# Optimization experiments

Hardware: AMD Instinct MI355X
Metric: run time of the kernel (lower is better)

Reference implementation:

```python
import jax, jax.numpy as jnp
import numpy as np

DT_RANK = 12


def _mixer(x, in_w, conv_w, conv_b, xproj_w, dt_w, dt_b, A_log, D_skip, out_w):
    # x: [B, L, d_model]
    B, L, _ = x.shape
    d_inner, d_state = A_log.shape
    k = conv_w.shape[-1]
    xz = x @ in_w.T                                  # [B, L, 2*d_inner]
    x_part, z = jnp.split(xz, 2, axis=-1)
    # causal depthwise conv1d (torch pads both sides with k-1 then slices [:L] == left-pad only)
    xc = x_part.transpose(0, 2, 1)                   # [B, d_inner, L]
    xc = jax.lax.conv_general_dilated(
        xc, conv_w, window_strides=(1,), padding=[(k - 1, 0)],
        feature_group_count=d_inner, dimension_numbers=("NCH", "OIH", "NCH"))
    xc = xc + conv_b[None, :, None]
    x_part = jax.nn.silu(xc.transpose(0, 2, 1))      # [B, L, d_inner]
    dt_bc = x_part @ xproj_w.T                       # [B, L, dt_rank + 2*d_state]
    dt_part = dt_bc[..., :DT_RANK]
    b_term = jnp.tanh(dt_bc[..., DT_RANK:DT_RANK + d_state])
    c_term = jnp.tanh(dt_bc[..., DT_RANK + d_state:])
    dt = jax.nn.softplus(dt_part @ dt_w.T + dt_b) + 1e-4   # [B, L, d_inner]
    a = -jnp.exp(A_log)                              # [d_inner, d_state]

    def step(state, inp):
        x_t, dt_t, b_t, c_t = inp                    # [B,di], [B,di], [B,N], [B,N]
        da = jnp.exp(dt_t[:, :, None] * a)           # [B, di, N]
        db = (1.0 - da) * b_t[:, None, :]
        state = da * state + db * x_t[:, :, None]
        y_t = (state * c_t[:, None, :]).sum(-1) + D_skip * x_t
        return state, y_t

    init = jnp.zeros((B, d_inner, d_state), x.dtype)
    xs = (x_part.transpose(1, 0, 2), dt.transpose(1, 0, 2),
          b_term.transpose(1, 0, 2), c_term.transpose(1, 0, 2))
    _, ys = jax.lax.scan(step, init, xs)             # ys: [L, B, d_inner]
    y = ys.transpose(1, 0, 2) * jax.nn.silu(z)
    return y @ out_w.T                               # [B, L, d_model]


def setup_inputs() -> dict:
    key = jax.random.key(0)
    B, L, D = 32, 577, 192
    d_inner, d_state, d_conv = 384, 8, 4
    ks = jax.random.split(key, 16)
    s = 0.02
    inp = {"x": jax.random.normal(ks[0], (B, L, D), jnp.float32)}
    for i, p in enumerate(["fw", "bw"]):
        kk = jax.random.split(ks[1 + i], 8)
        inp[f"{p}_in_w"] = jax.random.normal(kk[0], (2 * d_inner, D), jnp.float32) * s
        inp[f"{p}_conv_w"] = jax.random.normal(kk[1], (d_inner, 1, d_conv), jnp.float32) * 0.1
        inp[f"{p}_conv_b"] = jnp.zeros((d_inner,), jnp.float32)
        inp[f"{p}_xproj_w"] = jax.random.normal(kk[2], (DT_RANK + 2 * d_state, d_inner), jnp.float32) * s
        inp[f"{p}_dt_w"] = jax.random.normal(kk[3], (d_inner, DT_RANK), jnp.float32) * s
        inp[f"{p}_dt_b"] = jnp.zeros((d_inner,), jnp.float32)
        inp[f"{p}_A_log"] = jax.random.uniform(kk[4], (d_inner, d_state), jnp.float32)
        inp[f"{p}_D"] = jnp.ones((d_inner,), jnp.float32)
        inp[f"{p}_out_w"] = jax.random.normal(kk[5], (D, d_inner), jnp.float32) * s
    return inp


def reference(x,
              fw_in_w, fw_conv_w, fw_conv_b, fw_xproj_w, fw_dt_w, fw_dt_b, fw_A_log, fw_D, fw_out_w,
              bw_in_w, bw_conv_w, bw_conv_b, bw_xproj_w, bw_dt_w, bw_dt_b, bw_A_log, bw_D, bw_out_w):
    y_fwd = _mixer(x, fw_in_w, fw_conv_w, fw_conv_b, fw_xproj_w, fw_dt_w, fw_dt_b, fw_A_log, fw_D, fw_out_w)
    x_rev = jnp.flip(x, axis=1)
    y_bwd = _mixer(x_rev, bw_in_w, bw_conv_w, bw_conv_b, bw_xproj_w, bw_dt_w, bw_dt_b, bw_A_log, bw_D, bw_out_w)
    y_bwd = jnp.flip(y_bwd, axis=1)
    return 0.5 * (y_fwd + y_bwd)
```

## Files before the change

### kernel.cpp

```cpp
#include <hip/hip_runtime.h>
#include <hip/hip_bf16.h>

#define L2E 1.44269504088896340f
#define LN2 0.69314718055994531f

typedef __bf16 bf16x8 __attribute__((ext_vector_type(8)));
typedef __bf16 bf16x4 __attribute__((ext_vector_type(4)));
typedef float f32x4 __attribute__((ext_vector_type(4)));

__device__ __forceinline__ float fexp2(float x){ return __builtin_amdgcn_exp2f(x); }
__device__ __forceinline__ float flog2(float x){ return __builtin_amdgcn_logf(x); }
__device__ __forceinline__ float frcp(float x){ return __builtin_amdgcn_rcpf(x); }
__device__ __forceinline__ float fsigmoid(float x){ return frcp(1.f + fexp2(-x*L2E)); }
__device__ __forceinline__ float fsoftplus(float x){
  float sp = flog2(1.f + fexp2(x*L2E))*LN2;
  return (x > 15.f) ? x : sp;
}
__device__ __forceinline__ float ftanh_(float x){
  x = fminf(fmaxf(x, -10.f), 10.f);
  float e = fexp2(2.f*L2E*x);
  return (e - 1.f)*frcp(e + 1.f);
}

#define NB 32
#define LS 577
#define DM 192
#define DI 384
#define BL 18464
#define M2T 36928
#define T_CH 37
#define N_CH 16

__global__ __launch_bounds__(256) void k_prep(
    const float* __restrict__ x,
    const float* __restrict__ fw_in, const float* __restrict__ bw_in,
    const float* __restrict__ fw_out, const float* __restrict__ bw_out,
    const float* __restrict__ fw_xp, const float* __restrict__ bw_xp,
    const float* __restrict__ fw_al, const float* __restrict__ bw_al,
    __hip_bfloat16* __restrict__ xbf, __hip_bfloat16* __restrict__ wcat,
    __hip_bfloat16* __restrict__ wout, __hip_bfloat16* __restrict__ xpp,
    float* __restrict__ alog2)
{
  const int S0 = 3545088;
  const int S1 = S0 + 294912;
  const int S2 = S1 + 147456;
  const int S3 = S2 + 24576;
  const int S4 = S3 + 6144;
  int idx = blockIdx.x*256 + threadIdx.x;
  if (idx < S0) {
    xbf[idx] = __float2bfloat16(x[idx]);
  } else if (idx < S1) {
    int i = idx - S0; int r = i/192, k = i - r*192;
    float v = (r < 768) ? fw_in[r*192+k] : bw_in[(r-768)*192+k];
    wcat[i] = __float2bfloat16(v);
  } else if (idx < S2) {
    int i = idx - S1; int o = i/768, k = i - o*768;
    float v = 0.5f * ((k < 384) ? fw_out[o*384+k] : bw_out[o*384+(k-384)]);
    wout[i] = __float2bfloat16(v);
  } else if (idx < S3) {
    int i = idx - S2; int d = i/12288; int rr = i - d*12288;
    int n = rr/384, k = rr - n*384;
    const float* xp = d ? bw_xp : fw_xp;
    float v = (n < 28) ? xp[n*384+k] : 0.f;
    xpp[i] = __float2bfloat16(v);
  } else if (idx < S4) {
    int i = idx - S3;
    const float* al = (i < 3072) ? fw_al : bw_al;
    int j = (i < 3072) ? i : (i - 3072);
    alog2[i] = -fexp2(al[j]*L2E) * L2E;
  }
}

#define G1_LDA 104
#define G1_LDO 136
__global__ __launch_bounds__(256) void k_gemm1(const __hip_bfloat16* __restrict__ A,
                                               const __hip_bfloat16* __restrict__ Bw,
                                               __hip_bfloat16* __restrict__ xg,
                                               __hip_bfloat16* __restrict__ zsb)
{
  __shared__ __align__(16) __bf16 smem[26624];
  __bf16* ldsA = smem;
  __bf16* ldsB = smem + 128*G1_LDA;

  const int t = threadIdx.x;
  const int tm = blockIdx.x / 12, tn = blockIdx.x - tm*12;
  const int m0 = tm*128, n0 = tn*128;
  const int w = t >> 6, lane = t & 63;
  const int wr = (w >> 1)*64, wc = (w & 1)*64;
  const int r = lane & 15, q = lane >> 4;

  f32x4 acc[4][4];
  #pragma unroll
  for (int a=0;a<4;++a)
    #pragma unroll
    for (int b=0;b<4;++b) acc[a][b] = (f32x4){0.f,0.f,0.f,0.f};

  #pragma unroll
  for (int h=0; h<2; ++h) {
    if (h) __syncthreads();
    #pragma unroll
    for (int j=0;j<6;++j) {
      int cid = t + 256*j;
      int row = cid/12; int c8 = (cid - row*12)*8;
      int gr = m0 + row; if (gr > BL-1) gr = BL-1;
      bf16x8 va = *(const bf16x8*)(A + (size_t)gr*192 + h*96 + c8);
      *(bf16x8*)(ldsA + row*G1_LDA + c8) = va;
      bf16x8 vb = *(const bf16x8*)(Bw + (size_t)(n0+row)*192 + h*96 + c8);
      *(bf16x8*)(ldsB + row*G1_LDA + c8) = vb;
    }
    __syncthreads();
    #pragma unroll
    for (int kc=0; kc<96; kc+=32) {
      bf16x8 af[4], bfv[4];
      #pragma unroll
      for (int mi=0; mi<4; ++mi)
        af[mi] = *(const bf16x8*)(ldsA + (wr + mi*16 + r)*G1_LDA + q*8 + kc);
      #pragma unroll
      for (int ni=0; ni<4; ++ni)
        bfv[ni] = *(const bf16x8*)(ldsB + (wc + ni*16 + r)*G1_LDA + q*8 + kc);
      #pragma unroll
      for (int mi=0; mi<4; ++mi)
        #pragma unroll
        for (int ni=0; ni<4; ++ni)
          acc[mi][ni] = __builtin_amdgcn_mfma_f32_16x16x32_bf16(af[mi], bfv[ni], acc[mi][ni], 0,0,0);
    }
  }

  const int cat = tn/3;
  const int cbase = (tn - cat*3)*128;
  const int d = cat >> 1, isz = cat & 1;
  __syncthreads();
  __bf16* ldsO = smem;
  #pragma unroll
  for (int mi=0; mi<4; ++mi)
    #pragma unroll
    for (int ni=0; ni<4; ++ni)
      #pragma unroll
      for (int rg=0; rg<4; ++rg) {
        int row = wr + mi*16 + q*4 + rg;
        int col = wc + ni*16 + r;
        float v = acc[mi][ni][rg];
        if (isz) v = v * fsigmoid(v);
        ldsO[row*G1_LDO + col] = (__bf16)v;
      }
  __syncthreads();
  __hip_bfloat16* dst = (isz ? zsb : xg) + (size_t)(d*BL)*384 + cbase;
  const int c8 = (t & 15)*8;
  #pragma unroll
  for (int it=0; it<8; ++it) {
    int row = (t >> 4) + it*16;
    int grow = m0 + row;
    if (grow < BL) {
      bf16x8 v = *(const bf16x8*)(ldsO + row*G1_LDO + c8);
      *(bf16x8*)(dst + (size_t)grow*384 + c8) = v;
    }
  }
}

__global__ __launch_bounds__(256) void k_conv(const __hip_bfloat16* __restrict__ xg,
                                              __hip_bfloat16* __restrict__ xcs,
                                              const float* __restrict__ fw_cw, const float* __restrict__ fw_cb,
                                              const float* __restrict__ bw_cw, const float* __restrict__ bw_cb)
{
  int idx = blockIdx.x*256 + threadIdx.x;
  int token = idx / 96; int g = idx - token*96; int c0 = g*4;
  int d = token / BL; int r2 = token - d*BL;
  int b = r2 / LS; int i = r2 - b*LS;
  const float* cwp = (d ? bw_cw : fw_cw);
  const float* cbp = (d ? bw_cb : fw_cb);
  f32x4 w0 = *(const f32x4*)(cwp + (c0+0)*4);
  f32x4 w1 = *(const f32x4*)(cwp + (c0+1)*4);
  f32x4 w2 = *(const f32x4*)(cwp + (c0+2)*4);
  f32x4 w3 = *(const f32x4*)(cwp + (c0+3)*4);
  f32x4 accv = *(const f32x4*)(cbp + c0);
  const __hip_bfloat16* base = xg + ((size_t)(d*BL + b*LS))*384 + c0;
  #pragma unroll
  for (int j=0;j<4;++j) {
    int iw = d ? (i+3-j) : (i-3+j);
    bool valid = d ? (iw < LS) : (iw >= 0);
    if (valid) {
      bf16x4 xv = *(const bf16x4*)(base + (size_t)iw*384);
      f32x4 wj = (f32x4){w0[j], w1[j], w2[j], w3[j]};
      #pragma unroll
      for (int ch=0; ch<4; ++ch) accv[ch] += wj[ch]*(float)xv[ch];
    }
  }
  bf16x4 outv;
  #pragma unroll
  for (int ch=0; ch<4; ++ch) {
    float s = accv[ch]*fsigmoid(accv[ch]);
    outv[ch] = (__bf16)s;
  }
  *(bf16x4*)(xcs + (size_t)token*384 + c0) = outv;
}

__global__ __launch_bounds__(256) void k_dtbc(const __hip_bfloat16* __restrict__ A,
                                              const __hip_bfloat16* __restrict__ xpp,
                                              float* __restrict__ dtbc)
{
  const int wid = blockIdx.x*4 + (threadIdx.x >> 6);
  if (wid >= 1154) return;
  const int lane = threadIdx.x & 63;
  const int m0 = wid*32;
  const int r = lane & 15, q = lane >> 4;
  const int d = (m0 >= BL) ? 1 : 0;
  const __hip_bfloat16* Bp = xpp + (size_t)d*32*384;
  f32x4 acc[2][2];
  #pragma unroll
  for (int a=0;a<2;++a)
    #pragma unroll
    for (int b=0;b<2;++b) acc[a][b] = (f32x4){0.f,0.f,0.f,0.f};
  const __hip_bfloat16* Ab = A + (size_t)(m0 + r)*384 + q*8;
  const __hip_bfloat16* Bb = Bp + (size_t)r*384 + q*8;
  #pragma unroll
  for (int kc = 0; kc < 384; kc += 32) {
    bf16x8 af0 = *(const bf16x8*)(Ab + kc);
    bf16x8 af1 = *(const bf16x8*)(Ab + 16*384 + kc);
    bf16x8 bf0 = *(const bf16x8*)(Bb + kc);
    bf16x8 bf1 = *(const bf16x8*)(Bb + 16*384 + kc);
    acc[0][0] = __builtin_amdgcn_mfma_f32_16x16x32_bf16(af0, bf0, acc[0][0], 0,0,0);
    acc[0][1] = __builtin_amdgcn_mfma_f32_16x16x32_bf16(af0, bf1, acc[0][1], 0,0,0);
    acc[1][0] = __builtin_amdgcn_mfma_f32_16x16x32_bf16(af1, bf0, acc[1][0], 0,0,0);
    acc[1][1] = __builtin_amdgcn_mfma_f32_16x16x32_bf16(af1, bf1, acc[1][1], 0,0,0);
  }
  #pragma unroll
  for (int mi=0; mi<2; ++mi)
    #pragma unroll
    for (int ni=0; ni<2; ++ni)
      #pragma unroll
      for (int rg=0; rg<4; ++rg) {
        int n = ni*16 + r;
        if (n < 28) {
          int m = m0 + mi*16 + q*4 + rg;
          float v = acc[mi][ni][rg];
          if (n >= 12) v = ftanh_(v);
          int r2 = m - d*BL; int b = r2 / LS; int i = r2 - b*LS;
          int ts = d ? (LS-1-i) : i;
          dtbc[((size_t)((d*NB + b)*LS + ts))*28 + n] = v;
        }
      }
}

__global__ __launch_bounds__(256) void k_dtfull(const float* __restrict__ dtbc,
                                                const float* __restrict__ fw_dtw, const float* __restrict__ fw_dtb,
                                                const float* __restrict__ bw_dtw, const float* __restrict__ bw_dtb,
                                                float* __restrict__ dtf)
{
  int idx = blockIdx.x*256 + threadIdx.x;
  int m = idx / 384; int c = idx - m*384;
  int d = (m >= BL) ? 1 : 0;
  const float* dtw = (d ? bw_dtw : fw_dtw) + c*12;
  float dtr = (d ? bw_dtb : fw_dtb)[c];
  const float* dp = dtbc + (size_t)m*28;
  #pragma unroll
  for (int r=0;r<12;++r) dtr += dp[r]*dtw[r];
  dtf[idx] = fsoftplus(dtr) + 1e-4f;
}

__global__ __launch_bounds__(64) void k_scan1(const __hip_bfloat16* __restrict__ xcs,
                                              const float* __restrict__ dtbc,
                                              const float* __restrict__ dtf,
                                              const float* __restrict__ alog2,
                                              float* __restrict__ ps)
{
  __shared__ __align__(16) float sB[T_CH*8];
  const int bid = blockIdx.x;
  const int lane = threadIdx.x;
  const int kc = bid & 15; const int dbc = bid >> 4;
  const int cchunk = dbc % 6; const int db = dbc / 6;
  const int b = db & 31; const int d = db >> 5;
  const int c = cchunk*64 + lane;

  const int ts0 = kc*T_CH;
  const int ts1 = (ts0 + T_CH < LS) ? (ts0 + T_CH) : LS;

  {
    const float* src = dtbc + ((size_t)((d*NB+b)*LS + ts0))*28;
    int n4 = (ts1 - ts0)*2;
    for (int j = lane; j < n4; j += 64)
      *(f32x4*)(sB + j*4) = *(const f32x4*)(src + (size_t)(j>>1)*28 + 12 + (j&1)*4);
  }

  float al[8];
  const float* alp = alog2 + ((size_t)(d*384 + c))*8;
  #pragma unroll
  for (int s=0;s<8;++s) al[s] = alp[s];

  const __hip_bfloat16* xcb = xcs + ((size_t)(d*BL + b*LS))*384 + c;
  const float* dfb = dtf + ((size_t)((d*NB+b)*LS))*384 + c;

  float P[8], S[8];
  #pragma unroll
  for (int s=0;s<8;++s){ P[s]=1.f; S[s]=0.f; }

  __syncthreads();

  float xnb, dtn;
  {
    int i = d ? (LS-1-ts0) : ts0;
    xnb = __bfloat162float(xcb[(size_t)i*384]);
    dtn = dfb[(size_t)ts0*384];
  }
  for (int ts=ts0; ts<ts1; ++ts) {
    f32x4 B0 = *(const f32x4*)(sB + (ts-ts0)*8);
    f32x4 B1 = *(const f32x4*)(sB + (ts-ts0)*8 + 4);
    float xt = xnb, dt = dtn;
    if (ts+1 < ts1) {
      int i2 = d ? (LS-2-ts) : (ts+1);
      xnb = __bfloat162float(xcb[(size_t)i2*384]);
      dtn = dfb[(size_t)(ts+1)*384];
    }
    #pragma unroll
    for (int s=0;s<8;++s) {
      float da = fexp2(dt * al[s]);
      float Bv = (s<4) ? B0[s] : B1[s-4];
      float tmp = Bv*xt;
      S[s] = tmp + da*(S[s]-tmp);
      P[s] *= da;
    }
  }
  float* pp = ps + ((size_t)bid*16)*64 + lane;
  #pragma unroll
  for (int s=0;s<8;++s) pp[s*64] = P[s];
  #pragma unroll
  for (int s=0;s<8;++s) pp[(8+s)*64] = S[s];
}

__global__ __launch_bounds__(64) void k_comb(const float* __restrict__ ps,
                                             float* __restrict__ initst)
{
  const int dbc = blockIdx.x;
  const int lane = threadIdx.x;
  float st[8];
  #pragma unroll
  for (int s=0;s<8;++s) st[s]=0.f;
  for (int kc=0;kc<N_CH;++kc) {
    const float* pp = ps + ((size_t)(dbc*N_CH+kc)*16)*64 + lane;
    float* ip = initst + ((size_t)(dbc*N_CH+kc)*8)*64 + lane;
    #pragma unroll
    for (int s=0;s<8;++s) ip[s*64] = st[s];
    #pragma unroll
    for (int s=0;s<8;++s) {
      float P = pp[s*64], Sv = pp[(8+s)*64];
      st[s] = P*st[s] + Sv;
    }
  }
}

__global__ __launch_bounds__(64) void k_scan2(const __hip_bfloat16* __restrict__ xcs,
                                              const __hip_bfloat16* __restrict__ zsb,
                                              const float* __restrict__ dtbc,
                                              const float* __restrict__ dtf,
                                              const float* __restrict__ initst,
                                              const float* __restrict__ fw_D,
                                              const float* __restrict__ bw_D,
                                              const float* __restrict__ alog2,
                                              __hip_bfloat16* __restrict__ ybf)
{
  __shared__ __align__(16) float sBC[T_CH*16];
  const int bid = blockIdx.x;
  const int lane = threadIdx.x;
  const int kc = bid & 15; const int dbc = bid >> 4;
  const int cchunk = dbc % 6; const int db = dbc / 6;
  const int b = db & 31; const int d = db >> 5;
  const int c = cchunk*64 + lane;

  const int ts0 = kc*T_CH;
  const int ts1 = (ts0 + T_CH < LS) ? (ts0 + T_CH) : LS;

  {
    const float* src = dtbc + ((size_t)((d*NB+b)*LS + ts0))*28;
    int n4 = (ts1 - ts0)*4;
    for (int j = lane; j < n4; j += 64)
      *(f32x4*)(sBC + j*4) = *(const f32x4*)(src + (size_t)(j>>2)*28 + 12 + (j&3)*4);
  }

  const float Dc  = (d ? bw_D : fw_D)[c];
  float al[8];
  const float* alp = alog2 + ((size_t)(d*384 + c))*8;
  #pragma unroll
  for (int s=0;s<8;++s) al[s] = alp[s];

  float st[8];
  {
    const float* ip = initst + ((size_t)bid*8)*64 + lane;
    #pragma unroll
    for (int s=0;s<8;++s) st[s] = ip[s*64];
  }

  const __hip_bfloat16* xcb = xcs + ((size_t)(d*BL + b*LS))*384 + c;
  const __hip_bfloat16* zcb = zsb + ((size_t)(d*BL + b*LS))*384 + c;
  const float* dfb = dtf + ((size_t)((d*NB+b)*LS))*384 + c;
  __hip_bfloat16* ybase = ybf + (size_t)(b*LS)*768 + d*384 + c;

  __syncthreads();

  float xnb, znb, dtn;
  {
    int i = d ? (LS-1-ts0) : ts0;
    xnb = __bfloat162float(xcb[(size_t)i*384]);
    znb = __bfloat162float(zcb[(size_t)i*384]);
    dtn = dfb[(size_t)ts0*384];
  }
  for (int ts=ts0; ts<ts1; ++ts) {
    f32x4 B0 = *(const f32x4*)(sBC + (ts-ts0)*16);
    f32x4 B1 = *(const f32x4*)(sBC + (ts-ts0)*16 + 4);
    f32x4 C0 = *(const f32x4*)(sBC + (ts-ts0)*16 + 8);
    f32x4 C1 = *(const f32x4*)(sBC + (ts-ts0)*16 + 12);
    float xt = xnb, zs = znb, dt = dtn;
    int i = d ? (LS-1-ts) : ts;
    if (ts+1 < ts1) {
      int i2 = d ? (LS-2-ts) : (ts+1);
      xnb = __bfloat162float(xcb[(size_t)i2*384]);
      znb = __bfloat162float(zcb[(size_t)i2*384]);
      dtn = dfb[(size_t)(ts+1)*384];
    }
    float y = Dc * xt;
    #pragma unroll
    for (int s=0;s<8;++s) {
      float da = fexp2(dt * al[s]);
      float Bv = (s<4) ? B0[s] : B1[s-4];
      float Cv = (s<4) ? C0[s] : C1[s-4];
      float tmp = Bv*xt;
      st[s] = tmp + da*(st[s]-tmp);
      y += st[s]*Cv;
    }
    ybase[(size_t)i*768] = __float2bfloat16(y*zs);
  }
}

__global__ __launch_bounds__(256) void k_gemm2(const __hip_bfloat16* __restrict__ A,
                                               const __hip_bfloat16* __restrict__ Bw,
                                               float* __restrict__ C)
{
  const int wid = blockIdx.x*4 + (threadIdx.x >> 6);
  if (wid >= 1731) return;
  const int lane = threadIdx.x & 63;
  const int tm = wid / 3, tn = wid - tm*3;
  const int m0 = tm*32, n0 = tn*64;
  const int r = lane & 15, q = lane >> 4;
  f32x4 acc[2][4];
  #pragma unroll
  for (int a=0;a<2;++a)
    #pragma unroll
    for (int b=0;b<4;++b) acc[a][b] = (f32x4){0.f,0.f,0.f,0.f};
  const __hip_bfloat16* Ab = A + (size_t)(m0 + r)*768 + q*8;
  const __hip_bfloat16* Bb = Bw + (size_t)(n0 + r)*768 + q*8;
  #pragma unroll 4
  for (int kc = 0; kc < 768; kc += 32) {
    bf16x8 af0 = *(const bf16x8*)(Ab + kc);
    bf16x8 af1 = *(const bf16x8*)(Ab + 16*768 + kc);
    bf16x8 bf0 = *(const bf16x8*)(Bb + kc);
    bf16x8 bf1 = *(const bf16x8*)(Bb + 16*768 + kc);
    bf16x8 bf2 = *(const bf16x8*)(Bb + 32*768 + kc);
    bf16x8 bf3 = *(const bf16x8*)(Bb + 48*768 + kc);
    acc[0][0] = __builtin_amdgcn_mfma_f32_16x16x32_bf16(af0, bf0, acc[0][0], 0,0,0);
    acc[0][1] = __builtin_amdgcn_mfma_f32_16x16x32_bf16(af0, bf1, acc[0][1], 0,0,0);
    acc[0][2] = __builtin_amdgcn_mfma_f32_16x16x32_bf16(af0, bf2, acc[0][2], 0,0,0);
    acc[0][3] = __builtin_amdgcn_mfma_f32_16x16x32_bf16(af0, bf3, acc[0][3], 0,0,0);
    acc[1][0] = __builtin_amdgcn_mfma_f32_16x16x32_bf16(af1, bf0, acc[1][0], 0,0,0);
    acc[1][1] = __builtin_amdgcn_mfma_f32_16x16x32_bf16(af1, bf1, acc[1][1], 0,0,0);
    acc[1][2] = __builtin_amdgcn_mfma_f32_16x16x32_bf16(af1, bf2, acc[1][2], 0,0,0);
    acc[1][3] = __builtin_amdgcn_mfma_f32_16x16x32_bf16(af1, bf3, acc[1][3], 0,0,0);
  }
  #pragma unroll
  for (int mi=0; mi<2; ++mi)
    #pragma unroll
    for (int ni=0; ni<4; ++ni)
      #pragma unroll
      for (int rg=0; rg<4; ++rg) {
        int row = m0 + mi*16 + q*4 + rg;
        int col = n0 + ni*16 + r;
        C[(size_t)row*192 + col] = acc[mi][ni][rg];
      }
}

extern "C" void kernel_launch(void* const* d_in, const int* in_sizes, int n_in,
                              void* d_out, int out_size, void* d_ws, size_t ws_size,
                              hipStream_t stream) {
  const float* x        = (const float*)d_in[0];
  const float* fw_in_w  = (const float*)d_in[1];
  const float* fw_cw    = (const float*)d_in[2];
  const float* fw_cb    = (const float*)d_in[3];
  const float* fw_xp    = (const float*)d_in[4];
  const float* fw_dtw   = (const float*)d_in[5];
  const float* fw_dtb   = (const float*)d_in[6];
  const float* fw_al    = (const float*)d_in[7];
  const float* fw_D     = (const float*)d_in[8];
  const float* fw_ow    = (const float*)d_in[9];
  const float* bw_in_w  = (const float*)d_in[10];
  const float* bw_cw    = (const float*)d_in[11];
  const float* bw_cb    = (const float*)d_in[12];
  const float* bw_xp    = (const float*)d_in[13];
  const float* bw_dtw   = (const float*)d_in[14];
  const float* bw_dtb   = (const float*)d_in[15];
  const float* bw_al    = (const float*)d_in[16];
  const float* bw_D     = (const float*)d_in[17];
  const float* bw_ow    = (const float*)d_in[18];

  char* ws = (char*)d_ws;
  __hip_bfloat16* wcat = (__hip_bfloat16*)(ws + 0);
  __hip_bfloat16* wout = (__hip_bfloat16*)(ws + 589824);
  __hip_bfloat16* xpp  = (__hip_bfloat16*)(ws + 884736);
  float* alog2         = (float*)(ws + 933888);
  __hip_bfloat16* xbf  = (__hip_bfloat16*)(ws + 958464);
  __hip_bfloat16* xg   = (__hip_bfloat16*)(ws + 8048640);
  float* initst        = (float*)(ws + 8048640);
  __hip_bfloat16* zsb  = (__hip_bfloat16*)(ws + 36409344);
  __hip_bfloat16* xcs  = (__hip_bfloat16*)(ws + 64770048);
  float* dtbc          = (float*)(ws + 93130752);
  float* dtf           = (float*)(ws + 97266688);
  float* ps            = (float*)(ws + 153988096);
  __hip_bfloat16* ybf  = (__hip_bfloat16*)(ws + 153988096);

  hipLaunchKernelGGL(k_prep, dim3(15696), dim3(256), 0, stream,
                     x, fw_in_w, bw_in_w, fw_ow, bw_ow, fw_xp, bw_xp, fw_al, bw_al,
                     xbf, wcat, wout, xpp, alog2);
  hipLaunchKernelGGL(k_gemm1, dim3(1740), dim3(256), 0, stream, xbf, wcat, xg, zsb);
  hipLaunchKernelGGL(k_conv, dim3(13848), dim3(256), 0, stream,
                     xg, xcs, fw_cw, fw_cb, bw_cw, bw_cb);
  hipLaunchKernelGGL(k_dtbc, dim3(289), dim3(256), 0, stream, xcs, xpp, dtbc);
  hipLaunchKernelGGL(k_dtfull, dim3(55392), dim3(256), 0, stream,
                     dtbc, fw_dtw, fw_dtb, bw_dtw, bw_dtb, dtf);
  hipLaunchKernelGGL(k_scan1, dim3(6144), dim3(64), 0, stream,
                     xcs, dtbc, dtf, alog2, ps);
  hipLaunchKernelGGL(k_comb, dim3(384), dim3(64), 0, stream, ps, initst);
  hipLaunchKernelGGL(k_scan2, dim3(6144), dim3(64), 0, stream,
                     xcs, zsb, dtbc, dtf, initst, fw_D, bw_D, alog2, ybf);
  hipLaunchKernelGGL(k_gemm2, dim3(433), dim3(256), 0, stream, ybf, wout, (float*)d_out);
}
```

Before: 323.9 us.

## Stage output GEMM tiles in LDS and vectorize dt projection over four channels

The output GEMM now has each 256-thread block load a 64-row A tile and the full 192-row weight tile into LDS in 96-wide K slices. Four waves then compute a 32x96 sub-tile each from shared memory, instead of every wave streaming its own operands from global memory. The dt-projection kernel now has each thread produce four channels with vector loads, so the shared dtbc row is read once and the launch needs a quarter of the threads. The trade-off is fewer GEMM blocks (289) with more LDS use and block-level barriers, plus clamped loads and guarded stores for the partial last tile.

```diff
diff --git a/kernel.cpp b/kernel.cpp
--- a/kernel.cpp
+++ b/kernel.cpp
@@ -247,14 +247,31 @@
                                                 float* __restrict__ dtf)
 {
   int idx = blockIdx.x*256 + threadIdx.x;
-  int m = idx / 384; int c = idx - m*384;
+  int m = idx / 96; int g = idx - m*96; int c0 = g*4;
   int d = (m >= BL) ? 1 : 0;
-  const float* dtw = (d ? bw_dtw : fw_dtw) + c*12;
-  float dtr = (d ? bw_dtb : fw_dtb)[c];
+  const float* dtw = (d ? bw_dtw : fw_dtw);
+  const float* dtbp = (d ? bw_dtb : fw_dtb);
   const float* dp = dtbc + (size_t)m*28;
-  #pragma unroll
-  for (int r=0;r<12;++r) dtr += dp[r]*dtw[r];
-  dtf[idx] = fsoftplus(dtr) + 1e-4f;
+  f32x4 p0 = *(const f32x4*)(dp);
+  f32x4 p1 = *(const f32x4*)(dp+4);
+  f32x4 p2 = *(const f32x4*)(dp+8);
+  f32x4 acc = *(const f32x4*)(dtbp + c0);
+  #pragma unroll
+  for (int ch=0; ch<4; ++ch) {
+    const float* wv = dtw + (size_t)(c0+ch)*12;
+    f32x4 w0 = *(const f32x4*)(wv);
+    f32x4 w1 = *(const f32x4*)(wv+4);
+    f32x4 w2 = *(const f32x4*)(wv+8);
+    float s = acc[ch];
+    #pragma unroll
+    for (int r=0;r<4;++r) s += p0[r]*w0[r];
+    #pragma unroll
+    for (int r=0;r<4;++r) s += p1[r]*w1[r];
+    #pragma unroll
+    for (int r=0;r<4;++r) s += p2[r]*w2[r];
+    acc[ch] = fsoftplus(s) + 1e-4f;
+  }
+  *(f32x4*)(dtf + (size_t)m*384 + c0) = acc;
 }
 
 __global__ __launch_bounds__(64) void k_scan1(const __hip_bfloat16* __restrict__ xcs,
@@ -429,49 +446,70 @@
   }
 }
 
+#define G2_LDA 104
 __global__ __launch_bounds__(256) void k_gemm2(const __hip_bfloat16* __restrict__ A,
                                                const __hip_bfloat16* __restrict__ Bw,
                                                float* __restrict__ C)
 {
-  const int wid = blockIdx.x*4 + (threadIdx.x >> 6);
-  if (wid >= 1731) return;
-  const int lane = threadIdx.x & 63;
-  const int tm = wid / 3, tn = wid - tm*3;
-  const int m0 = tm*32, n0 = tn*64;
+  __shared__ __align__(16) __bf16 smem[26624];
+  __bf16* ldsA = smem;
+  __bf16* ldsB = smem + 64*G2_LDA;
+
+  const int t = threadIdx.x;
+  const int m0 = blockIdx.x*64;
+  const int w = t >> 6, lane = t & 63;
+  const int wr = (w >> 1)*32, wc = (w & 1)*96;
   const int r = lane & 15, q = lane >> 4;
-  f32x4 acc[2][4];
+
+  f32x4 acc[2][6];
   #pragma unroll
   for (int a=0;a<2;++a)
     #pragma unroll
-    for (int b=0;b<4;++b) acc[a][b] = (f32x4){0.f,0.f,0.f,0.f};
-  const __hip_bfloat16* Ab = A + (size_t)(m0 + r)*768 + q*8;
-  const __hip_bfloat16* Bb = Bw + (size_t)(n0 + r)*768 + q*8;
-  #pragma unroll 4
-  for (int kc = 0; kc < 768; kc += 32) {
-    bf16x8 af0 = *(const bf16x8*)(Ab + kc);
-    bf16x8 af1 = *(const bf16x8*)(Ab + 16*768 + kc);
-    bf16x8 bf0 = *(const bf16x8*)(Bb + kc);
-    bf16x8 bf1 = *(const bf16x8*)(Bb + 16*768 + kc);
-    bf16x8 bf2 = *(const bf16x8*)(Bb + 32*768 + kc);
-    bf16x8 bf3 = *(const bf16x8*)(Bb + 48*768 + kc);
-    acc[0][0] = __builtin_amdgcn_mfma_f32_16x16x32_bf16(af0, bf0, acc[0][0], 0,0,0);
-    acc[0][1] = __builtin_amdgcn_mfma_f32_16x16x32_bf16(af0, bf1, acc[0][1], 0,0,0);
-    acc[0][2] = __builtin_amdgcn_mfma_f32_16x16x32_bf16(af0, bf2, acc[0][2], 0,0,0);
-    acc[0][3] = __builtin_amdgcn_mfma_f32_16x16x32_bf16(af0, bf3, acc[0][3], 0,0,0);
-    acc[1][0] = __builtin_amdgcn_mfma_f32_16x16x32_bf16(af1, bf0, acc[1][0], 0,0,0);
-    acc[1][1] = __builtin_amdgcn_mfma_f32_16x16x32_bf16(af1, bf1, acc[1][1], 0,0,0);
-    acc[1][2] = __builtin_amdgcn_mfma_f32_16x16x32_bf16(af1, bf2, acc[1][2], 0,0,0);
-    acc[1][3] = __builtin_amdgcn_mfma_f32_16x16x32_bf16(af1, bf3, acc[1][3], 0,0,0);
-  }
+    for (int b=0;b<6;++b) acc[a][b] = (f32x4){0.f,0.f,0.f,0.f};
+
+  #pragma unroll 1
+  for (int h=0; h<8; ++h) {
+    if (h) __syncthreads();
+    #pragma unroll
+    for (int j=0;j<3;++j) {
+      int cid = t + 256*j;
+      int row = cid/12; int c8 = (cid - row*12)*8;
+      int gr = m0 + row; if (gr > BL-1) gr = BL-1;
+      *(bf16x8*)(ldsA + row*G2_LDA + c8) = *(const bf16x8*)(A + (size_t)gr*768 + h*96 + c8);
+    }
+    #pragma unroll
+    for (int j=0;j<9;++j) {
+      int cid = t + 256*j;
+      int row = cid/12; int c8 = (cid - row*12)*8;
+      *(bf16x8*)(ldsB + row*G2_LDA + c8) = *(const bf16x8*)(Bw + (size_t)row*768 + h*96 + c8);
+    }
+    __syncthreads();
+    #pragma unroll
+    for (int kc=0; kc<96; kc+=32) {
+      bf16x8 af[2], bfv[6];
+      #pragma unroll
+      for (int mi=0; mi<2; ++mi)
+        af[mi] = *(const bf16x8*)(ldsA + (wr + mi*16 + r)*G2_LDA + q*8 + kc);
+      #pragma unroll
+      for (int ni=0; ni<6; ++ni)
+        bfv[ni] = *(const bf16x8*)(ldsB + (wc + ni*16 + r)*G2_LDA + q*8 + kc);
+      #pragma unroll
+      for (int mi=0; mi<2; ++mi)
+        #pragma unroll
+        for (int ni=0; ni<6; ++ni)
+          acc[mi][ni] = __builtin_amdgcn_mfma_f32_16x16x32_bf16(af[mi], bfv[ni], acc[mi][ni], 0,0,0);
+    }
+  }
+
   #pragma unroll
   for (int mi=0; mi<2; ++mi)
     #pragma unroll
-    for (int ni=0; ni<4; ++ni)
+    for (int ni=0; ni<6; ++ni)
       #pragma unroll
       for (int rg=0; rg<4; ++rg) {
-        int row = m0 + mi*16 + q*4 + rg;
-        int col = n0 + ni*16 + r;
-        C[(size_t)row*192 + col] = acc[mi][ni][rg];
+        int row = m0 + wr + mi*16 + q*4 + rg;
+        int col = wc + ni*16 + r;
+        if (row < BL) C[(size_t)row*192 + col] = acc[mi][ni][rg];
       }
 }
 
@@ -520,12 +558,12 @@
   hipLaunchKernelGGL(k_conv, dim3(13848), dim3(256), 0, stream,
                      xg, xcs, fw_cw, fw_cb, bw_cw, bw_cb);
   hipLaunchKernelGGL(k_dtbc, dim3(289), dim3(256), 0, stream, xcs, xpp, dtbc);
-  hipLaunchKernelGGL(k_dtfull, dim3(55392), dim3(256), 0, stream,
+  hipLaunchKernelGGL(k_dtfull, dim3(13848), dim3(256), 0, stream,
                      dtbc, fw_dtw, fw_dtb, bw_dtw, bw_dtb, dtf);
   hipLaunchKernelGGL(k_scan1, dim3(6144), dim3(64), 0, stream,
                      xcs, dtbc, dtf, alog2, ps);
   hipLaunchKernelGGL(k_comb, dim3(384), dim3(64), 0, stream, ps, initst);
   hipLaunchKernelGGL(k_scan2, dim3(6144), dim3(64), 0, stream,
                      xcs, zsb, dtbc, dtf, initst, fw_D, bw_D, alog2, ybf);
-  hipLaunchKernelGGL(k_gemm2, dim3(433), dim3(256), 0, stream, ybf, wout, (float*)d_out);
-}
+  hipLaunchKernelGGL(k_gemm2, dim3(289), dim3(256), 0, stream, ybf, wout, (float*)d_out);
+}
```

After: 308.9 us. -4.6%, faster.
